# Optimization experiments

Measured on AMD Instinct MI355X. Metric: run time of the kernel, lower is better.

## Reference

```python
import jax, jax.numpy as jnp
import numpy as np

B_SCALE = 1.3195079565048218  # per_level_scale
N_LEVELS = 4                  # kernel hardcodes 4 levels
F = 4                         # kernel hardcodes 4 features per level
BASE = 32.0                   # kernel hardcodes base resolution 32
MAX_PARAMS = 2 ** 19
N_POINTS = 2097152


def _level_meta():
    offsets = []
    off = 0
    for i in range(N_LEVELS):
        res = int(np.ceil(BASE * np.exp(i * np.log(B_SCALE)) - 1.0)) + 1
        p = res ** 3
        p = p if p % 8 == 0 else ((p + 7) // 8) * 8
        p = min(MAX_PARAMS, p)
        offsets.append(off)
        off += p
    return offsets, off

OFFSETS, TOTAL_PARAMS = _level_meta()
TOTAL_HASH_SIZE = TOTAL_PARAMS * F  # 2772480


def setup_inputs() -> dict:
    key = jax.random.key(0)
    k1, k2 = jax.random.split(key)
    # scale to [0, 0.9) so all 8 corner indices stay inside each level's grid
    positions = jax.random.uniform(k1, (N_POINTS, 3), dtype=jnp.float32) * 0.9
    # original init: uniform(-1e-4, 1e-4); small random values
    table = jax.random.normal(k2, (TOTAL_HASH_SIZE,), dtype=jnp.float32) * 1e-4
    return {"positions": positions, "table": table}


def _encode(positions, table):
    tab = table.reshape(-1, F)  # [total_params, 4]
    n = positions.shape[0]
    outs = []
    for level in range(N_LEVELS):
        scale = BASE * (B_SCALE ** level) - 1.0
        res = int(np.ceil(scale)) + 1
        pos = positions * scale + 0.5            # [n,3]
        grid = jnp.floor(pos)
        frac = pos - grid                         # trilinear fractions
        grid = grid.astype(jnp.int32)
        acc = jnp.zeros((n, F), positions.dtype)
        for c in range(8):  # 8 corners of the cell
            w = jnp.ones((n,), positions.dtype)
            idx = jnp.zeros((n,), jnp.int32)
            stride = 1
            for d in range(3):
                if (c >> d) & 1:
                    coord = grid[:, d] + 1
                    w = w * frac[:, d]
                else:
                    coord = grid[:, d]
                    w = w * (1.0 - frac[:, d])
                idx = idx + coord * stride
                stride *= res
            acc = acc + w[:, None] * tab[OFFSETS[level] + idx]
        outs.append(acc)
    return jnp.concatenate(outs, axis=1)  # [n, 16]


def reference(positions, table):
    return _encode(positions, table)
```

## Files before the change

### kernel.cpp

```cpp
#include <hip/hip_runtime.h>
#include <math.h>


#define NBINS        512
#define BIN_SCALE    (8.0f / 0.9f)
#define PTS_PER_BLK  2048
#define SCAT_ITERS   (PTS_PER_BLK / 256)
#define CAP          4608

#define ENC_THREADS  512
#define ENC_BPB      (CAP / ENC_THREADS)

#define D1 7
#define D2 9
#define D3 11
#define A1 0
#define A2 (A1 + D1*D1*D1)
#define A3 (A2 + D2*D2*D2)
#define LDS_TOT (A3 + D3*D3*D3)

typedef float vfloat4 __attribute__((ext_vector_type(4)));

__device__ __forceinline__ int bin_of(float x, float y, float z) {
    int bx = (int)(x * BIN_SCALE); bx = bx < 0 ? 0 : (bx > 7 ? 7 : bx);
    int by = (int)(y * BIN_SCALE); by = by < 0 ? 0 : (by > 7 ? 7 : by);
    int bz = (int)(z * BIN_SCALE); bz = bz < 0 ? 0 : (bz > 7 ? 7 : bz);
    return bx | (by << 3) | (bz << 6);
}


__global__ __launch_bounds__(512) void init_cursor_kernel(int* __restrict__ cursor)
{
    int t = threadIdx.x;
    cursor[t] = t * CAP;
}

__global__ __launch_bounds__(256) void scatter_cap_kernel(
    const float* __restrict__ pos, int n, int* __restrict__ cursor,
    float4* __restrict__ sorted)
{
    __shared__ int lds_hist[NBINS];
    __shared__ int lds_base[NBINS];
    int tid = threadIdx.x;
    long base = (long)blockIdx.x * PTS_PER_BLK;
    lds_hist[tid] = 0; lds_hist[tid + 256] = 0;
    __syncthreads();

    float px[SCAT_ITERS], py[SCAT_ITERS], pz[SCAT_ITERS];
    int br[SCAT_ITERS];
#pragma unroll
    for (int j = 0; j < SCAT_ITERS; ++j) {
        long p = base + j * 256 + tid;
        int packed = -1;
        if (p < n) {
            float x = pos[3 * p], y = pos[3 * p + 1], z = pos[3 * p + 2];
            px[j] = x; py[j] = y; pz[j] = z;
            int b = bin_of(x, y, z);
            int r = atomicAdd(&lds_hist[b], 1);
            packed = (r << 9) | b;
        }
        br[j] = packed;
    }
    __syncthreads();
    int c0 = lds_hist[tid];       if (c0) lds_base[tid]       = atomicAdd(&cursor[tid], c0);
    int c1 = lds_hist[tid + 256]; if (c1) lds_base[tid + 256] = atomicAdd(&cursor[tid + 256], c1);
    __syncthreads();

#pragma unroll
    for (int j = 0; j < SCAT_ITERS; ++j) {
        if (br[j] < 0) continue;
        long p = base + j * 256 + tid;
        int b = br[j] & (NBINS - 1);
        int r = br[j] >> 9;
        sorted[lds_base[b] + r] =
            make_float4(px[j], py[j], pz[j], __int_as_float((int)p));
    }
}

template<int D>
__device__ __forceinline__ void stage_win(
    float4* __restrict__ dst, const float4* __restrict__ tab,
    int off, int res, int Bx, int By, int Bz, int tid)
{
    const int DD = D * D, DDD = D * D * D;
    for (int e = tid; e < DDD; e += ENC_THREADS) {
        int iz  = e / DD;
        int rem = e - iz * DD;
        int iy  = rem / D;
        int ix  = rem - iy * D;
        int gx = Bx + ix; gx = gx < 0 ? 0 : (gx > res - 1 ? res - 1 : gx);
        int gy = By + iy; gy = gy < 0 ? 0 : (gy > res - 1 ? res - 1 : gy);
        int gz = Bz + iz; gz = gz < 0 ? 0 : (gz > res - 1 ? res - 1 : gz);
        dst[e] = tab[off + gx + gy * res + gz * res * res];
    }
}

__device__ __forceinline__ float4 interp_global(
    const float4* __restrict__ tab,
    float x, float y, float z, float scale, int res, int off)
{
    float hx = x * scale + 0.5f, hy = y * scale + 0.5f, hz = z * scale + 0.5f;
    float fx = floorf(hx), fy = floorf(hy), fz = floorf(hz);
    float wx = hx - fx, wy = hy - fy, wz = hz - fz;
    float ox = 1.0f - wx, oy = 1.0f - wy, oz = 1.0f - wz;
    int res2  = res * res;
    int basei = off + (int)fx + (int)fy * res + (int)fz * res2;
    float4 acc = make_float4(0.f, 0.f, 0.f, 0.f);
#pragma unroll
    for (int c = 0; c < 8; ++c) {
        int   idx = basei + ((c & 1) ? 1 : 0) + ((c & 2) ? res : 0) + ((c & 4) ? res2 : 0);
        float w   = ((c & 1) ? wx : ox) * ((c & 2) ? wy : oy) * ((c & 4) ? wz : oz);
        float4 v  = tab[idx];
        acc.x += w * v.x; acc.y += w * v.y; acc.z += w * v.z; acc.w += w * v.w;
    }
    return acc;
}

template<int D>
__device__ __forceinline__ float4 interp_one(
    const float4* __restrict__ lds, const float4* __restrict__ tab,
    float x, float y, float z, float scale, int res, int off,
    int Bx, int By, int Bz)
{
    float hx = x * scale + 0.5f, hy = y * scale + 0.5f, hz = z * scale + 0.5f;
    float fx = floorf(hx), fy = floorf(hy), fz = floorf(hz);
    float wx = hx - fx, wy = hy - fy, wz = hz - fz;
    float ox = 1.0f - wx, oy = 1.0f - wy, oz = 1.0f - wz;
    int gx = (int)fx, gy = (int)fy, gz = (int)fz;
    int lx = gx - Bx, ly = gy - By, lz = gz - Bz;
    float4 acc = make_float4(0.f, 0.f, 0.f, 0.f);
    if ((unsigned)lx <= (unsigned)(D - 2) &&
        (unsigned)ly <= (unsigned)(D - 2) &&
        (unsigned)lz <= (unsigned)(D - 2)) {
        int basei = (lz * D + ly) * D + lx;
#pragma unroll
        for (int c = 0; c < 8; ++c) {
            int   idx = basei + ((c & 1) ? 1 : 0) + ((c & 2) ? D : 0) + ((c & 4) ? D * D : 0);
            float w   = ((c & 1) ? wx : ox) * ((c & 2) ? wy : oy) * ((c & 4) ? wz : oz);
            float4 v  = lds[idx];
            acc.x += w * v.x; acc.y += w * v.y; acc.z += w * v.z; acc.w += w * v.w;
        }
    } else {
        int res2  = res * res;
        int basei = off + gx + gy * res + gz * res2;
#pragma unroll
        for (int c = 0; c < 8; ++c) {
            int   idx = basei + ((c & 1) ? 1 : 0) + ((c & 2) ? res : 0) + ((c & 4) ? res2 : 0);
            float w   = ((c & 1) ? wx : ox) * ((c & 2) ? wy : oy) * ((c & 4) ? wz : oz);
            float4 v  = tab[idx];
            acc.x += w * v.x; acc.y += w * v.y; acc.z += w * v.z; acc.w += w * v.w;
        }
    }
    return acc;
}

__global__ __launch_bounds__(ENC_THREADS) void encode_cap_lds_kernel(
    const float4* __restrict__ sorted,
    const int* __restrict__ cursor,
    const float4* __restrict__ tab,
    float4* __restrict__ out,
    float s0, float s1, float s2, float s3,
    int r0, int r1, int r2, int r3,
    int o0, int o1, int o2, int o3)
{
    __shared__ float4 lds[LDS_TOT];

    int nb = (int)gridDim.x;
    int lb = (int)blockIdx.x;
    lb = (lb & 7) * (nb >> 3) + (lb >> 3);

    int b   = lb / ENC_BPB;
    int k   = lb - b * ENC_BPB;
    int cnt = cursor[b] - b * CAP;
    if (k * ENC_THREADS >= cnt) return;

    int tid = threadIdx.x;

    int local = k * ENC_THREADS + tid;
    int j = b * CAP + local;
    vfloat4 rv = __builtin_nontemporal_load((const vfloat4*)&sorted[j]);

    int bx = b & 7, by = (b >> 3) & 7, bz = b >> 6;
    float lox = bx * 0.1125f, loy = by * 0.1125f, loz = bz * 0.1125f;

    int B1x = (int)floorf(lox * s1 + 0.5f), B1y = (int)floorf(loy * s1 + 0.5f), B1z = (int)floorf(loz * s1 + 0.5f);
    int B2x = (int)floorf(lox * s2 + 0.5f), B2y = (int)floorf(loy * s2 + 0.5f), B2z = (int)floorf(loz * s2 + 0.5f);
    int B3x = (int)floorf(lox * s3 + 0.5f), B3y = (int)floorf(loy * s3 + 0.5f), B3z = (int)floorf(loz * s3 + 0.5f);

    stage_win<D1>(lds + A1, tab, o1, r1, B1x, B1y, B1z, tid);
    stage_win<D2>(lds + A2, tab, o2, r2, B2x, B2y, B2z, tid);
    stage_win<D3>(lds + A3, tab, o3, r3, B3x, B3y, B3z, tid);
    __syncthreads();

    if (local >= cnt) return;

    float x = rv.x, y = rv.y, z = rv.z;
    int p = __float_as_int(rv.w);
    float4* op = out + (long)p * 4;

    float4 a0 = interp_global(tab, x, y, z, s0, r0, o0);
    op[0] = a0;
    float4 a1 = interp_one<D1>(lds + A1, tab, x, y, z, s1, r1, o1, B1x, B1y, B1z);
    op[1] = a1;
    float4 a2 = interp_one<D2>(lds + A2, tab, x, y, z, s2, r2, o2, B2x, B2y, B2z);
    op[2] = a2;
    float4 a3 = interp_one<D3>(lds + A3, tab, x, y, z, s3, r3, o3, B3x, B3y, B3z);
    op[3] = a3;
}


__device__ __forceinline__ void interp_levels(
    float4 rec, const float4* __restrict__ tab, float4* __restrict__ o,
    float s0, float s1, float s2, float s3,
    int r0, int r1, int r2, int r3,
    int o0, int o1, int o2, int o3)
{
    float scales[4] = { s0, s1, s2, s3 };
    int   ress[4]   = { r0, r1, r2, r3 };
    int   offs[4]   = { o0, o1, o2, o3 };
#pragma unroll
    for (int l = 0; l < 4; ++l) {
        float scale = scales[l];
        int   res   = ress[l];
        int   off   = offs[l];
        float hx = rec.x * scale + 0.5f;
        float hy = rec.y * scale + 0.5f;
        float hz = rec.z * scale + 0.5f;
        float gx = floorf(hx), gy = floorf(hy), gz = floorf(hz);
        float wx = hx - gx,   wy = hy - gy,   wz = hz - gz;
        float ox = 1.0f - wx, oy = 1.0f - wy, oz = 1.0f - wz;
        int res2 = res * res;
        int base = off + (int)gx + (int)gy * res + (int)gz * res2;
        float4 acc = make_float4(0.f, 0.f, 0.f, 0.f);
#pragma unroll
        for (int c = 0; c < 8; ++c) {
            int   idx = base + ((c & 1) ? 1 : 0) + ((c & 2) ? res : 0) + ((c & 4) ? res2 : 0);
            float w   = ((c & 1) ? wx : ox) * ((c & 2) ? wy : oy) * ((c & 4) ? wz : oz);
            float4 v  = tab[idx];
            acc.x += w * v.x; acc.y += w * v.y; acc.z += w * v.z; acc.w += w * v.w;
        }
        o[l] = acc;
    }
}


__global__ __launch_bounds__(256) void hist_kernel(
    const float* __restrict__ pos, int n, int* __restrict__ hist)
{
    __shared__ int lh[NBINS];
    int tid = threadIdx.x;
    lh[tid] = 0; lh[tid + 256] = 0;
    __syncthreads();
    long base = (long)blockIdx.x * PTS_PER_BLK;
#pragma unroll
    for (int j = 0; j < SCAT_ITERS; ++j) {
        long p = base + j * 256 + tid;
        if (p < n) {
            float x = pos[3 * p], y = pos[3 * p + 1], z = pos[3 * p + 2];
            atomicAdd(&lh[bin_of(x, y, z)], 1);
        }
    }
    __syncthreads();
    int c0 = lh[tid];       if (c0) atomicAdd(&hist[tid], c0);
    int c1 = lh[tid + 256]; if (c1) atomicAdd(&hist[tid + 256], c1);
}

__global__ __launch_bounds__(256) void scan_kernel(
    const int* __restrict__ hist, int* __restrict__ cursor)
{
    __shared__ int partials[256];
    int t = threadIdx.x;
    int a = hist[2 * t], b = hist[2 * t + 1];
    int sum = a + b;
    partials[t] = sum;
    __syncthreads();
    for (int off = 1; off < 256; off <<= 1) {
        int v = (t >= off) ? partials[t - off] : 0;
        __syncthreads();
        partials[t] += v;
        __syncthreads();
    }
    int base = partials[t] - sum;
    cursor[2 * t]     = base;
    cursor[2 * t + 1] = base + a;
}

__global__ __launch_bounds__(256) void encode_kernel(
    const float4* __restrict__ sorted, const float4* __restrict__ tab,
    float4* __restrict__ out, int n,
    float s0, float s1, float s2, float s3,
    int r0, int r1, int r2, int r3,
    int o0, int o1, int o2, int o3)
{
    int j = blockIdx.x * blockDim.x + threadIdx.x;
    if (j >= n) return;
    vfloat4 rv = __builtin_nontemporal_load((const vfloat4*)&sorted[j]);
    float4 rec = make_float4(rv.x, rv.y, rv.z, rv.w);
    int p = __float_as_int(rec.w);
    interp_levels(rec, tab, out + (long)p * 4,
                  s0, s1, s2, s3, r0, r1, r2, r3, o0, o1, o2, o3);
}

__global__ __launch_bounds__(256) void encode_direct_kernel(
    const float* __restrict__ pos, const float4* __restrict__ tab,
    float4* __restrict__ out, int n_points,
    float s0, float s1, float s2, float s3,
    int r0, int r1, int r2, int r3,
    int o0, int o1, int o2, int o3)
{
    int t = blockIdx.x * blockDim.x + threadIdx.x;
    int p = t >> 2;
    if (p >= n_points) return;
    int l = t & 3;
    float scale = (l == 0) ? s0 : (l == 1) ? s1 : (l == 2) ? s2 : s3;
    int   res   = (l == 0) ? r0 : (l == 1) ? r1 : (l == 2) ? r2 : r3;
    int   off   = (l == 0) ? o0 : (l == 1) ? o1 : (l == 2) ? o2 : o3;
    float px = pos[3 * p], py = pos[3 * p + 1], pz = pos[3 * p + 2];
    float hx = px * scale + 0.5f, hy = py * scale + 0.5f, hz = pz * scale + 0.5f;
    float gx = floorf(hx), gy = floorf(hy), gz = floorf(hz);
    float wx = hx - gx, wy = hy - gy, wz = hz - gz;
    float ox = 1.f - wx, oy = 1.f - wy, oz = 1.f - wz;
    int res2 = res * res;
    int base = off + (int)gx + (int)gy * res + (int)gz * res2;
    float4 acc = make_float4(0.f, 0.f, 0.f, 0.f);
#pragma unroll
    for (int c = 0; c < 8; ++c) {
        int   idx = base + ((c & 1) ? 1 : 0) + ((c & 2) ? res : 0) + ((c & 4) ? res2 : 0);
        float w   = ((c & 1) ? wx : ox) * ((c & 2) ? wy : oy) * ((c & 4) ? wz : oz);
        float4 v  = tab[idx];
        acc.x += w * v.x; acc.y += w * v.y; acc.z += w * v.z; acc.w += w * v.w;
    }
    out[t] = acc;
}

extern "C" void kernel_launch(void* const* d_in, const int* in_sizes, int n_in,
                              void* d_out, int out_size, void* d_ws, size_t ws_size,
                              hipStream_t stream) {
    const float*  positions = (const float*)d_in[0];
    const float4* table     = (const float4*)d_in[1];
    float4*       out       = (float4*)d_out;
    int n = in_sizes[0] / 3;

    const double B_SCALE = 1.3195079565048218;
    const double BASE = 32.0;
    const long   MAX_PARAMS = 1L << 19;
    float scales[4]; int res[4], offs[4];
    long off = 0;
    for (int l = 0; l < 4; ++l) {
        double s = BASE * pow(B_SCALE, (double)l) - 1.0;
        scales[l] = (float)s;
        int r = (int)ceil(s) + 1;
        res[l] = r;
        offs[l] = (int)off;
        long pcount = (long)r * r * r;
        if (pcount % 8 != 0) pcount = (pcount + 7) / 8 * 8;
        if (pcount > MAX_PARAMS) pcount = MAX_PARAMS;
        off += pcount;
    }

    int block = 256;
    size_t need_cap   = (size_t)NBINS * sizeof(int) + (size_t)NBINS * CAP * 16;
    size_t need_exact = (size_t)NBINS * sizeof(int) * 2 + (size_t)n * 16;

    if (ws_size >= need_cap && n <= NBINS * (CAP - 512)) {
        int*    cursor = (int*)d_ws;
        float4* sorted = (float4*)(cursor + NBINS);

        int grid_pts = (n + PTS_PER_BLK - 1) / PTS_PER_BLK;
        int grid_enc = NBINS * ENC_BPB;

        init_cursor_kernel<<<1, NBINS, 0, stream>>>(cursor);
        scatter_cap_kernel<<<grid_pts, block, 0, stream>>>(positions, n, cursor, sorted);
        encode_cap_lds_kernel<<<grid_enc, ENC_THREADS, 0, stream>>>(
            sorted, cursor, table, out,
            scales[0], scales[1], scales[2], scales[3],
            res[0], res[1], res[2], res[3],
            offs[0], offs[1], offs[2], offs[3]);
    } else if (ws_size >= need_exact) {
        int*    hist   = (int*)d_ws;
        int*    cursor = hist + NBINS;
        float4* sorted = (float4*)(cursor + NBINS);

        int grid_pts = (n + PTS_PER_BLK - 1) / PTS_PER_BLK;
        int grid_enc = (n + block - 1) / block;

        (void)hipMemsetAsync(hist, 0, NBINS * sizeof(int), stream);
        hist_kernel<<<grid_pts, block, 0, stream>>>(positions, n, hist);
        scan_kernel<<<1, 256, 0, stream>>>(hist, cursor);
        scatter_cap_kernel<<<grid_pts, block, 0, stream>>>(positions, n, cursor, sorted);
        encode_kernel<<<grid_enc, block, 0, stream>>>(
            sorted, table, out, n,
            scales[0], scales[1], scales[2], scales[3],
            res[0], res[1], res[2], res[3],
            offs[0], offs[1], offs[2], offs[3]);
    } else {
        long n_threads = 4L * n;
        long grid = (n_threads + block - 1) / block;
        encode_direct_kernel<<<dim3((unsigned)grid), dim3(block), 0, stream>>>(
            positions, table, out, n,
            scales[0], scales[1], scales[2], scales[3],
            res[0], res[1], res[2], res[3],
            offs[0], offs[1], offs[2], offs[3]);
    }
}
```

Before: 258.0 us.

## Process two points per encode thread and widen scatter blocks to 512 threads

The encode kernel now handles up to 1024 points per block, two per thread, so each staged LDS window of table entries is reused by twice as many points and fewer blocks repeat the staging. The scatter and histogram kernels move to 512 threads with 4096 points per block, which halves the number of global cursor atomics. The cursor init kernel is replaced by a memset, and bin offsets are now added inside scatter. Each encode thread carries more registers, and fewer encode blocks may lower occupancy or load balance.

```diff
diff --git a/kernel.cpp b/kernel.cpp
--- a/kernel.cpp
+++ b/kernel.cpp
@@ -4,12 +4,14 @@
 
 #define NBINS        512
 #define BIN_SCALE    (8.0f / 0.9f)
-#define PTS_PER_BLK  2048
-#define SCAT_ITERS   (PTS_PER_BLK / 256)
+#define SCAT_THREADS 512
+#define PTS_PER_BLK  4096
+#define SCAT_ITERS   (PTS_PER_BLK / SCAT_THREADS)
 #define CAP          4608
 
 #define ENC_THREADS  512
-#define ENC_BPB      (CAP / ENC_THREADS)
+#define ENC_PPB      1024
+#define ENC_BPB      ((CAP + ENC_PPB - 1) / ENC_PPB)
 
 #define D1 7
 #define D2 9
@@ -29,28 +31,22 @@
 }
 
 
-__global__ __launch_bounds__(512) void init_cursor_kernel(int* __restrict__ cursor)
-{
-    int t = threadIdx.x;
-    cursor[t] = t * CAP;
-}
-
-__global__ __launch_bounds__(256) void scatter_cap_kernel(
+__global__ __launch_bounds__(SCAT_THREADS) void scatter_cap_kernel(
     const float* __restrict__ pos, int n, int* __restrict__ cursor,
-    float4* __restrict__ sorted)
+    float4* __restrict__ sorted, int bin_stride)
 {
     __shared__ int lds_hist[NBINS];
     __shared__ int lds_base[NBINS];
     int tid = threadIdx.x;
     long base = (long)blockIdx.x * PTS_PER_BLK;
-    lds_hist[tid] = 0; lds_hist[tid + 256] = 0;
+    lds_hist[tid] = 0;
     __syncthreads();
 
     float px[SCAT_ITERS], py[SCAT_ITERS], pz[SCAT_ITERS];
     int br[SCAT_ITERS];
 #pragma unroll
     for (int j = 0; j < SCAT_ITERS; ++j) {
-        long p = base + j * 256 + tid;
+        long p = base + j * SCAT_THREADS + tid;
         int packed = -1;
         if (p < n) {
             float x = pos[3 * p], y = pos[3 * p + 1], z = pos[3 * p + 2];
@@ -62,18 +58,18 @@
         br[j] = packed;
     }
     __syncthreads();
-    int c0 = lds_hist[tid];       if (c0) lds_base[tid]       = atomicAdd(&cursor[tid], c0);
-    int c1 = lds_hist[tid + 256]; if (c1) lds_base[tid + 256] = atomicAdd(&cursor[tid + 256], c1);
+    int c = lds_hist[tid];
+    if (c) lds_base[tid] = atomicAdd(&cursor[tid], c);
     __syncthreads();
 
 #pragma unroll
     for (int j = 0; j < SCAT_ITERS; ++j) {
         if (br[j] < 0) continue;
-        long p = base + j * 256 + tid;
+        long p = base + j * SCAT_THREADS + tid;
         int b = br[j] & (NBINS - 1);
         int r = br[j] >> 9;
-        sorted[lds_base[b] + r] =
-            make_float4(px[j], py[j], pz[j], __int_as_float((int)p));
+        long slot = (long)b * bin_stride + lds_base[b] + r;
+        sorted[slot] = make_float4(px[j], py[j], pz[j], __int_as_float((int)p));
     }
 }
 
@@ -171,14 +167,17 @@
 
     int b   = lb / ENC_BPB;
     int k   = lb - b * ENC_BPB;
-    int cnt = cursor[b] - b * CAP;
-    if (k * ENC_THREADS >= cnt) return;
+    int cnt = cursor[b];
+    if (k * ENC_PPB >= cnt) return;
 
     int tid = threadIdx.x;
 
-    int local = k * ENC_THREADS + tid;
-    int j = b * CAP + local;
-    vfloat4 rv = __builtin_nontemporal_load((const vfloat4*)&sorted[j]);
+    int la  = k * ENC_PPB + tid;
+    int lb2 = la + ENC_THREADS;
+    int ja  = b * CAP + la;
+    int jb  = b * CAP + (lb2 < CAP ? lb2 : (CAP - 1));
+    vfloat4 ra = __builtin_nontemporal_load((const vfloat4*)&sorted[ja]);
+    vfloat4 rb = __builtin_nontemporal_load((const vfloat4*)&sorted[jb]);
 
     int bx = b & 7, by = (b >> 3) & 7, bz = b >> 6;
     float lox = bx * 0.1125f, loy = by * 0.1125f, loz = bz * 0.1125f;
@@ -192,20 +191,36 @@
     stage_win<D3>(lds + A3, tab, o3, r3, B3x, B3y, B3z, tid);
     __syncthreads();
 
-    if (local >= cnt) return;
-
-    float x = rv.x, y = rv.y, z = rv.z;
-    int p = __float_as_int(rv.w);
-    float4* op = out + (long)p * 4;
-
-    float4 a0 = interp_global(tab, x, y, z, s0, r0, o0);
-    op[0] = a0;
-    float4 a1 = interp_one<D1>(lds + A1, tab, x, y, z, s1, r1, o1, B1x, B1y, B1z);
-    op[1] = a1;
-    float4 a2 = interp_one<D2>(lds + A2, tab, x, y, z, s2, r2, o2, B2x, B2y, B2z);
-    op[2] = a2;
-    float4 a3 = interp_one<D3>(lds + A3, tab, x, y, z, s3, r3, o3, B3x, B3y, B3z);
-    op[3] = a3;
+    bool va = la < cnt, vb = lb2 < cnt;
+    if (!va && !vb) return;
+
+    float cx = lox + 0.05625f, cy = loy + 0.05625f, cz = loz + 0.05625f;
+    float xa = va ? ra.x : cx, ya = va ? ra.y : cy, za = va ? ra.z : cz;
+    float xb = vb ? rb.x : cx, yb = vb ? rb.y : cy, zb = vb ? rb.z : cz;
+    long pa = va ? (long)__float_as_int(ra.w) : 0;
+    long pb = vb ? (long)__float_as_int(rb.w) : 0;
+    float4* oa = out + pa * 4;
+    float4* ob = out + pb * 4;
+
+    float4 A0 = interp_global(tab, xa, ya, za, s0, r0, o0);
+    float4 B0 = interp_global(tab, xb, yb, zb, s0, r0, o0);
+    if (va) oa[0] = A0;
+    if (vb) ob[0] = B0;
+
+    float4 Al1 = interp_one<D1>(lds + A1, tab, xa, ya, za, s1, r1, o1, B1x, B1y, B1z);
+    float4 Bl1 = interp_one<D1>(lds + A1, tab, xb, yb, zb, s1, r1, o1, B1x, B1y, B1z);
+    if (va) oa[1] = Al1;
+    if (vb) ob[1] = Bl1;
+
+    float4 Al2 = interp_one<D2>(lds + A2, tab, xa, ya, za, s2, r2, o2, B2x, B2y, B2z);
+    float4 Bl2 = interp_one<D2>(lds + A2, tab, xb, yb, zb, s2, r2, o2, B2x, B2y, B2z);
+    if (va) oa[2] = Al2;
+    if (vb) ob[2] = Bl2;
+
+    float4 Al3 = interp_one<D3>(lds + A3, tab, xa, ya, za, s3, r3, o3, B3x, B3y, B3z);
+    float4 Bl3 = interp_one<D3>(lds + A3, tab, xb, yb, zb, s3, r3, o3, B3x, B3y, B3z);
+    if (va) oa[3] = Al3;
+    if (vb) ob[3] = Bl3;
 }
 
 
@@ -244,25 +259,25 @@
 }
 
 
-__global__ __launch_bounds__(256) void hist_kernel(
+__global__ __launch_bounds__(SCAT_THREADS) void hist_kernel(
     const float* __restrict__ pos, int n, int* __restrict__ hist)
 {
     __shared__ int lh[NBINS];
     int tid = threadIdx.x;
-    lh[tid] = 0; lh[tid + 256] = 0;
+    lh[tid] = 0;
     __syncthreads();
     long base = (long)blockIdx.x * PTS_PER_BLK;
 #pragma unroll
     for (int j = 0; j < SCAT_ITERS; ++j) {
-        long p = base + j * 256 + tid;
+        long p = base + j * SCAT_THREADS + tid;
         if (p < n) {
             float x = pos[3 * p], y = pos[3 * p + 1], z = pos[3 * p + 2];
             atomicAdd(&lh[bin_of(x, y, z)], 1);
         }
     }
     __syncthreads();
-    int c0 = lh[tid];       if (c0) atomicAdd(&hist[tid], c0);
-    int c1 = lh[tid + 256]; if (c1) atomicAdd(&hist[tid + 256], c1);
+    int c = lh[tid];
+    if (c) atomicAdd(&hist[tid], c);
 }
 
 __global__ __launch_bounds__(256) void scan_kernel(
@@ -358,7 +373,6 @@
         off += pcount;
     }
 
-    int block = 256;
     size_t need_cap   = (size_t)NBINS * sizeof(int) + (size_t)NBINS * CAP * 16;
     size_t need_exact = (size_t)NBINS * sizeof(int) * 2 + (size_t)n * 16;
 
@@ -369,8 +383,9 @@
         int grid_pts = (n + PTS_PER_BLK - 1) / PTS_PER_BLK;
         int grid_enc = NBINS * ENC_BPB;
 
-        init_cursor_kernel<<<1, NBINS, 0, stream>>>(cursor);
-        scatter_cap_kernel<<<grid_pts, block, 0, stream>>>(positions, n, cursor, sorted);
+        (void)hipMemsetAsync(cursor, 0, NBINS * sizeof(int), stream);
+        scatter_cap_kernel<<<grid_pts, SCAT_THREADS, 0, stream>>>(
+            positions, n, cursor, sorted, CAP);
         encode_cap_lds_kernel<<<grid_enc, ENC_THREADS, 0, stream>>>(
             sorted, cursor, table, out,
             scales[0], scales[1], scales[2], scales[3],
@@ -382,21 +397,22 @@
         float4* sorted = (float4*)(cursor + NBINS);
 
         int grid_pts = (n + PTS_PER_BLK - 1) / PTS_PER_BLK;
-        int grid_enc = (n + block - 1) / block;
+        int grid_enc = (n + 255) / 256;
 
         (void)hipMemsetAsync(hist, 0, NBINS * sizeof(int), stream);
-        hist_kernel<<<grid_pts, block, 0, stream>>>(positions, n, hist);
+        hist_kernel<<<grid_pts, SCAT_THREADS, 0, stream>>>(positions, n, hist);
         scan_kernel<<<1, 256, 0, stream>>>(hist, cursor);
-        scatter_cap_kernel<<<grid_pts, block, 0, stream>>>(positions, n, cursor, sorted);
-        encode_kernel<<<grid_enc, block, 0, stream>>>(
+        scatter_cap_kernel<<<grid_pts, SCAT_THREADS, 0, stream>>>(
+            positions, n, cursor, sorted, 0);
+        encode_kernel<<<grid_enc, 256, 0, stream>>>(
             sorted, table, out, n,
             scales[0], scales[1], scales[2], scales[3],
             res[0], res[1], res[2], res[3],
             offs[0], offs[1], offs[2], offs[3]);
     } else {
         long n_threads = 4L * n;
-        long grid = (n_threads + block - 1) / block;
-        encode_direct_kernel<<<dim3((unsigned)grid), dim3(block), 0, stream>>>(
+        long grid = (n_threads + 255) / 256;
+        encode_direct_kernel<<<dim3((unsigned)grid), dim3(256), 0, stream>>>(
             positions, table, out, n,
             scales[0], scales[1], scales[2], scales[3],
             res[0], res[1], res[2], res[3],
```

New measurement: 261.4 us. No clear change (+1.3%).

## Stage scatter output in LDS sorted by bin for coalesced global writes

Applied to the files above, without the earlier changes.

The scatter kernel now runs 512 threads over 4096 points per block. It computes a block-local prefix scan over bin counts and places records into LDS in bin order, then writes them out contiguously so that global stores to each bin's region are coalesced instead of scattered. Cursors now hold per-bin counts, zeroed with a memset instead of an init kernel, and the bin stride is passed as a parameter. The cost is a 512-step LDS scan with many barriers and about 75KB of LDS per block, which lowers occupancy.

```diff
diff --git a/kernel.cpp b/kernel.cpp
--- a/kernel.cpp
+++ b/kernel.cpp
@@ -4,8 +4,9 @@
 
 #define NBINS        512
 #define BIN_SCALE    (8.0f / 0.9f)
-#define PTS_PER_BLK  2048
-#define SCAT_ITERS   (PTS_PER_BLK / 256)
+#define SCAT_THREADS 512
+#define PTS_PER_BLK  4096
+#define SCAT_ITERS   (PTS_PER_BLK / SCAT_THREADS)
 #define CAP          4608
 
 #define ENC_THREADS  512
@@ -29,28 +30,26 @@
 }
 
 
-__global__ __launch_bounds__(512) void init_cursor_kernel(int* __restrict__ cursor)
-{
-    int t = threadIdx.x;
-    cursor[t] = t * CAP;
-}
-
-__global__ __launch_bounds__(256) void scatter_cap_kernel(
+__global__ __launch_bounds__(SCAT_THREADS) void scatter_cap_kernel(
     const float* __restrict__ pos, int n, int* __restrict__ cursor,
-    float4* __restrict__ sorted)
-{
+    float4* __restrict__ sorted, int bin_stride)
+{
+    __shared__ float4         lds_rec[PTS_PER_BLK];
+    __shared__ unsigned short lds_bin[PTS_PER_BLK];
     __shared__ int lds_hist[NBINS];
-    __shared__ int lds_base[NBINS];
+    __shared__ int lds_lbase[NBINS];
+    __shared__ int lds_gbase[NBINS];
+
     int tid = threadIdx.x;
     long base = (long)blockIdx.x * PTS_PER_BLK;
-    lds_hist[tid] = 0; lds_hist[tid + 256] = 0;
+    lds_hist[tid] = 0;
     __syncthreads();
 
     float px[SCAT_ITERS], py[SCAT_ITERS], pz[SCAT_ITERS];
     int br[SCAT_ITERS];
 #pragma unroll
     for (int j = 0; j < SCAT_ITERS; ++j) {
-        long p = base + j * 256 + tid;
+        long p = base + j * SCAT_THREADS + tid;
         int packed = -1;
         if (p < n) {
             float x = pos[3 * p], y = pos[3 * p + 1], z = pos[3 * p + 2];
@@ -62,18 +61,41 @@
         br[j] = packed;
     }
     __syncthreads();
-    int c0 = lds_hist[tid];       if (c0) lds_base[tid]       = atomicAdd(&cursor[tid], c0);
-    int c1 = lds_hist[tid + 256]; if (c1) lds_base[tid + 256] = atomicAdd(&cursor[tid + 256], c1);
+
+    int cntb = lds_hist[tid];
+    lds_lbase[tid] = cntb;
+    __syncthreads();
+    for (int off = 1; off < NBINS; off <<= 1) {
+        int v = (tid >= off) ? lds_lbase[tid - off] : 0;
+        __syncthreads();
+        lds_lbase[tid] += v;
+        __syncthreads();
+    }
+    int excl = lds_lbase[tid] - cntb;
+    if (cntb) lds_gbase[tid] = atomicAdd(&cursor[tid], cntb);
+    lds_lbase[tid] = excl;
     __syncthreads();
 
 #pragma unroll
     for (int j = 0; j < SCAT_ITERS; ++j) {
         if (br[j] < 0) continue;
-        long p = base + j * 256 + tid;
         int b = br[j] & (NBINS - 1);
         int r = br[j] >> 9;
-        sorted[lds_base[b] + r] =
-            make_float4(px[j], py[j], pz[j], __int_as_float((int)p));
+        int s = lds_lbase[b] + r;
+        long p = base + j * SCAT_THREADS + tid;
+        lds_rec[s] = make_float4(px[j], py[j], pz[j], __int_as_float((int)p));
+        lds_bin[s] = (unsigned short)b;
+    }
+    __syncthreads();
+
+    long rem = (long)n - base;
+    int tot = rem >= PTS_PER_BLK ? PTS_PER_BLK : (rem > 0 ? (int)rem : 0);
+    for (int s = tid; s < tot; s += SCAT_THREADS) {
+        float4 rec = lds_rec[s];
+        int b = lds_bin[s];
+        int off_in_bin = s - lds_lbase[b];
+        long slot = (long)b * bin_stride + lds_gbase[b] + off_in_bin;
+        sorted[slot] = rec;
     }
 }
 
@@ -171,7 +193,7 @@
 
     int b   = lb / ENC_BPB;
     int k   = lb - b * ENC_BPB;
-    int cnt = cursor[b] - b * CAP;
+    int cnt = cursor[b];
     if (k * ENC_THREADS >= cnt) return;
 
     int tid = threadIdx.x;
@@ -244,25 +266,25 @@
 }
 
 
-__global__ __launch_bounds__(256) void hist_kernel(
+__global__ __launch_bounds__(SCAT_THREADS) void hist_kernel(
     const float* __restrict__ pos, int n, int* __restrict__ hist)
 {
     __shared__ int lh[NBINS];
     int tid = threadIdx.x;
-    lh[tid] = 0; lh[tid + 256] = 0;
+    lh[tid] = 0;
     __syncthreads();
     long base = (long)blockIdx.x * PTS_PER_BLK;
 #pragma unroll
     for (int j = 0; j < SCAT_ITERS; ++j) {
-        long p = base + j * 256 + tid;
+        long p = base + j * SCAT_THREADS + tid;
         if (p < n) {
             float x = pos[3 * p], y = pos[3 * p + 1], z = pos[3 * p + 2];
             atomicAdd(&lh[bin_of(x, y, z)], 1);
         }
     }
     __syncthreads();
-    int c0 = lh[tid];       if (c0) atomicAdd(&hist[tid], c0);
-    int c1 = lh[tid + 256]; if (c1) atomicAdd(&hist[tid + 256], c1);
+    int c = lh[tid];
+    if (c) atomicAdd(&hist[tid], c);
 }
 
 __global__ __launch_bounds__(256) void scan_kernel(
@@ -358,7 +380,6 @@
         off += pcount;
     }
 
-    int block = 256;
     size_t need_cap   = (size_t)NBINS * sizeof(int) + (size_t)NBINS * CAP * 16;
     size_t need_exact = (size_t)NBINS * sizeof(int) * 2 + (size_t)n * 16;
 
@@ -369,8 +390,9 @@
         int grid_pts = (n + PTS_PER_BLK - 1) / PTS_PER_BLK;
         int grid_enc = NBINS * ENC_BPB;
 
-        init_cursor_kernel<<<1, NBINS, 0, stream>>>(cursor);
-        scatter_cap_kernel<<<grid_pts, block, 0, stream>>>(positions, n, cursor, sorted);
+        (void)hipMemsetAsync(cursor, 0, NBINS * sizeof(int), stream);
+        scatter_cap_kernel<<<grid_pts, SCAT_THREADS, 0, stream>>>(
+            positions, n, cursor, sorted, CAP);
         encode_cap_lds_kernel<<<grid_enc, ENC_THREADS, 0, stream>>>(
             sorted, cursor, table, out,
             scales[0], scales[1], scales[2], scales[3],
@@ -382,21 +404,22 @@
         float4* sorted = (float4*)(cursor + NBINS);
 
         int grid_pts = (n + PTS_PER_BLK - 1) / PTS_PER_BLK;
-        int grid_enc = (n + block - 1) / block;
+        int grid_enc = (n + 255) / 256;
 
         (void)hipMemsetAsync(hist, 0, NBINS * sizeof(int), stream);
-        hist_kernel<<<grid_pts, block, 0, stream>>>(positions, n, hist);
+        hist_kernel<<<grid_pts, SCAT_THREADS, 0, stream>>>(positions, n, hist);
         scan_kernel<<<1, 256, 0, stream>>>(hist, cursor);
-        scatter_cap_kernel<<<grid_pts, block, 0, stream>>>(positions, n, cursor, sorted);
-        encode_kernel<<<grid_enc, block, 0, stream>>>(
+        scatter_cap_kernel<<<grid_pts, SCAT_THREADS, 0, stream>>>(
+            positions, n, cursor, sorted, 0);
+        encode_kernel<<<grid_enc, 256, 0, stream>>>(
             sorted, table, out, n,
             scales[0], scales[1], scales[2], scales[3],
             res[0], res[1], res[2], res[3],
             offs[0], offs[1], offs[2], offs[3]);
     } else {
         long n_threads = 4L * n;
-        long grid = (n_threads + block - 1) / block;
-        encode_direct_kernel<<<dim3((unsigned)grid), dim3(block), 0, stream>>>(
+        long grid = (n_threads + 255) / 256;
+        encode_direct_kernel<<<dim3((unsigned)grid), dim3(256), 0, stream>>>(
             positions, table, out, n,
             scales[0], scales[1], scales[2], scales[3],
             res[0], res[1], res[2], res[3],
```

After: 242.0 us. -6.2%, faster.
